# Kernel optimization log

Measured on AMD Instinct MI355X. Metric: run time of the kernel, lower is better.

The kernel has to match this reference:

```python
import jax, jax.numpy as jnp
import numpy as np

REG = 0.1
NITER = 30
EPS = 1e-10

def _encode(x, W1, b1, W2, b2):
    # (B, N, D) -> (B, N, H), MLP applied pointwise
    h = jax.nn.relu(jnp.einsum('bnd,dh->bnh', x, W1) + b1)
    return jnp.einsum('bnh,he->bne', h, W2) + b2

def _l2_normalize(x):
    n = jnp.linalg.norm(x, axis=-1, keepdims=True)
    return x / jnp.maximum(n, 1e-12)

def setup_inputs() -> dict:
    key = jax.random.key(0)
    ks = jax.random.split(key, 6)
    B, N, D, H, E = 32, 1024, 128, 512, 256
    A_batch = jax.random.normal(ks[0], (B, N, D), dtype=jnp.float32)
    B_batch = jax.random.normal(ks[1], (B, N, D), dtype=jnp.float32)
    mask = jnp.ones((B, N), dtype=bool)
    W1 = jax.random.normal(ks[2], (D, H), dtype=jnp.float32) * (1.0 / np.sqrt(D))
    b1 = jnp.zeros((H,), dtype=jnp.float32)
    W2 = jax.random.normal(ks[3], (H, E), dtype=jnp.float32) * (1.0 / np.sqrt(H))
    b2 = jnp.zeros((E,), dtype=jnp.float32)
    return {"A_batch": A_batch, "B_batch": B_batch, "mask": mask,
            "W1": W1, "b1": b1, "W2": W2, "b2": b2}

def reference(A_batch, B_batch, mask, W1, b1, W2, b2):
    A_emb = _l2_normalize(_encode(A_batch, W1, b1, W2, b2))  # (B,N,E)
    B_emb = _l2_normalize(_encode(B_batch, W1, b1, W2, b2))  # (B,M,E)
    C = 1.0 - jnp.einsum('bne,bme->bnm', A_emb, B_emb)       # (B,N,M)
    K = jnp.exp(-C / REG)
    m = mask.astype(jnp.float32)                             # (B,N)
    lengths = m.sum(axis=1)[:, None, None]                   # (B,1,1)
    u_target = m[:, :, None] / lengths                       # (B,N,1)
    v_target = m[:, :, None] / lengths                       # (B,M,1)
    K = K * (m[:, :, None] * m[:, None, :])                  # masked kernel

    def body(_, uv):
        u, v = uv
        u = u_target / (jnp.einsum('bnm,bmk->bnk', K, v) + EPS)
        v = v_target / (jnp.einsum('bnm,bnk->bmk', K, u) + EPS)
        return (u, v)

    u, v = jax.lax.fori_loop(0, NITER, body, (u_target, v_target))
    T = u * K * jnp.swapaxes(v, 1, 2)                        # (B,N,M)
    cost = jnp.sum(T * C, axis=(1, 2))                       # (B,)
    return cost
```

## Files before the change

kernel.cpp:

```cpp
#include <hip/hip_runtime.h>
#include <hip/hip_bf16.h>

namespace {
constexpr int NB = 32;
constexpr int NN = 1024;
constexpr int ND = 128;
constexpr int NH = 512;
constexpr int NE = 256;
constexpr float FEPS = 1e-10f;
}

typedef short bf16x8v __attribute__((ext_vector_type(8)));
typedef unsigned short u16x8 __attribute__((ext_vector_type(8)));
typedef float f32x4 __attribute__((ext_vector_type(4)));
typedef float f32x2 __attribute__((ext_vector_type(2)));

__device__ __forceinline__ unsigned short bf16_rne(float x) {
  unsigned int u = __float_as_uint(x);
  u += 0x7FFFu + ((u >> 16) & 1u);
  return (unsigned short)(u >> 16);
}
__device__ __forceinline__ float bf2f(unsigned short h) {
  return __uint_as_float((unsigned int)h << 16);
}

__device__ __forceinline__ unsigned char f2f8(float x) {
  unsigned short u = __builtin_bit_cast(unsigned short, (_Float16)x);
  u = (unsigned short)(u + 0x7Fu + ((u >> 8) & 1u));
  return (unsigned char)(u >> 8);
}
__device__ __forceinline__ float f8tof(unsigned int b) {
  return (float)__builtin_bit_cast(_Float16, (unsigned short)(b << 8));
}

#if __has_builtin(__builtin_amdgcn_cvt_pk_f32_bf8)
#define DEC8(DST, D) {                                                          \
    f32x2 p_;                                                                   \
    p_ = __builtin_amdgcn_cvt_pk_f32_bf8((int)(D).x, false); (DST)[0] = p_.x; (DST)[1] = p_.y; \
    p_ = __builtin_amdgcn_cvt_pk_f32_bf8((int)(D).x, true);  (DST)[2] = p_.x; (DST)[3] = p_.y; \
    p_ = __builtin_amdgcn_cvt_pk_f32_bf8((int)(D).y, false); (DST)[4] = p_.x; (DST)[5] = p_.y; \
    p_ = __builtin_amdgcn_cvt_pk_f32_bf8((int)(D).y, true);  (DST)[6] = p_.x; (DST)[7] = p_.y; \
  }
#else
#define DEC8(DST, D) {                                                          \
    (DST)[0] = f8tof((D).x & 255u);         (DST)[1] = f8tof(((D).x >> 8) & 255u);  \
    (DST)[2] = f8tof(((D).x >> 16) & 255u); (DST)[3] = f8tof((D).x >> 24);          \
    (DST)[4] = f8tof((D).y & 255u);         (DST)[5] = f8tof(((D).y >> 8) & 255u);  \
    (DST)[6] = f8tof(((D).y >> 16) & 255u); (DST)[7] = f8tof((D).y >> 24);          \
  }
#endif

__global__ void k_prep_w(const float* __restrict__ W1, const float* __restrict__ W2,
                         unsigned short* __restrict__ W1f, unsigned short* __restrict__ W2f,
                         float* __restrict__ zbase)
{
  const int t = blockIdx.x * blockDim.x + threadIdx.x;
  for (int i = t; i < 31 * NB * NN; i += 768 * 256) zbase[i] = 0.f;

  if (t < 128 * 512) {
    const int j = t & 7, l = (t >> 3) & 63, ks = (t >> 9) & 3, ct = t >> 11;
    const int k = ks * 32 + ((l >> 4) << 3) + j;
    const int n = (ct << 4) + (l & 15);
    W1f[t] = bf16_rne(W1[k * NH + n]);
  } else {
    const int t2 = t - 128 * 512;
    const int j = t2 & 7, l = (t2 >> 3) & 63, ks = (t2 >> 9) & 15, ct = t2 >> 13;
    const int k = ks * 32 + ((l >> 4) << 3) + j;
    const int n = (ct << 4) + (l & 15);
    W2f[t2] = bf16_rne(W2[k * NE + n]);
  }
}

__global__ __launch_bounds__(256) void k_encode_mfma(
    const float* __restrict__ Ain, const float* __restrict__ Bin,
    const unsigned short* __restrict__ W1f, const float* __restrict__ b1,
    const unsigned short* __restrict__ W2f, const float* __restrict__ b2,
    unsigned short* __restrict__ Aemb, unsigned short* __restrict__ Bemb)
{
  __shared__ __align__(16) char smem[81920];
  const int tid = threadIdx.x;
  const int lane = tid & 63;
  const int w = tid >> 6;
  const int g0 = blockIdx.x * 64;
  const float* src; unsigned short* dst; int r0;
  if (g0 < NB * NN) { src = Ain; dst = Aemb; r0 = g0; }
  else              { src = Bin; dst = Bemb; r0 = g0 - NB * NN; }

  {
    const int row = tid >> 2;
    const int q = tid & 3;
    const float* xr = src + (size_t)(r0 + row) * ND + q * 32;
    const int rx = (row & 7) << 4;
#pragma unroll
    for (int uq = 0; uq < 4; ++uq) {
      const float4 f0 = *(const float4*)(xr + uq * 8);
      const float4 f1 = *(const float4*)(xr + uq * 8 + 4);
      u16x8 p;
      p[0] = bf16_rne(f0.x); p[1] = bf16_rne(f0.y); p[2] = bf16_rne(f0.z); p[3] = bf16_rne(f0.w);
      p[4] = bf16_rne(f1.x); p[5] = bf16_rne(f1.y); p[6] = bf16_rne(f1.z); p[7] = bf16_rne(f1.w);
      const int byte = (row * 256 + q * 64 + uq * 16) ^ rx;
      *(u16x8*)(smem + byte) = p;
    }
  }
  __syncthreads();

  bf16x8v xa[4];
  {
    const int r = w * 16 + (lane & 15);
    const int rx = (r & 7) << 4;
#pragma unroll
    for (int ks = 0; ks < 4; ++ks) {
      const int byte = (r * 256 + ks * 64 + ((lane >> 4) << 4)) ^ rx;
      xa[ks] = *(const bf16x8v*)(smem + byte);
    }
  }

  const bf16x8v* W1v = (const bf16x8v*)W1f;
  const bf16x8v* W2v = (const bf16x8v*)W2f;
  char* Hbase = smem + 16384;

#pragma unroll
  for (int ct = 0; ct < 32; ct += 2) {
    f32x4 a0 = {0.f, 0.f, 0.f, 0.f};
    f32x4 a1 = {0.f, 0.f, 0.f, 0.f};
#pragma unroll
    for (int ks = 0; ks < 4; ++ks) {
      const bf16x8v wb0 = W1v[((ct << 2) + ks) * 64 + lane];
      const bf16x8v wb1 = W1v[(((ct + 1) << 2) + ks) * 64 + lane];
      a0 = __builtin_amdgcn_mfma_f32_16x16x32_bf16(xa[ks], wb0, a0, 0, 0, 0);
      a1 = __builtin_amdgcn_mfma_f32_16x16x32_bf16(xa[ks], wb1, a1, 0, 0, 0);
    }
    const int c0 = (ct << 4) + (lane & 15);
    const float bv0 = b1[c0];
    const float bv1 = b1[c0 + 16];
    const int rbase = w * 16 + ((lane >> 4) << 2);
#pragma unroll
    for (int reg = 0; reg < 4; ++reg) {
      const int r = rbase + reg;
      const int rx = (r & 7) << 4;
      const float h0 = fmaxf(a0[reg] + bv0, 0.f);
      const float h1 = fmaxf(a1[reg] + bv1, 0.f);
      *(unsigned short*)(Hbase + ((r * 1024 + c0 * 2) ^ rx)) = bf16_rne(h0);
      *(unsigned short*)(Hbase + ((r * 1024 + (c0 + 16) * 2) ^ rx)) = bf16_rne(h1);
    }
  }
  __syncthreads();

  bf16x8v ha[16];
  {
    const int r = w * 16 + (lane & 15);
    const int rx = (r & 7) << 4;
#pragma unroll
    for (int ks = 0; ks < 16; ++ks) {
      const int byte = (r * 1024 + ks * 64 + ((lane >> 4) << 4)) ^ rx;
      ha[ks] = *(const bf16x8v*)(Hbase + byte);
    }
  }

  f32x4 acc[16];
#pragma unroll
  for (int ct = 0; ct < 16; ct += 2) {
    f32x4 a0 = {0.f, 0.f, 0.f, 0.f};
    f32x4 a1 = {0.f, 0.f, 0.f, 0.f};
#pragma unroll
    for (int ks = 0; ks < 16; ++ks) {
      const bf16x8v wb0 = W2v[((ct << 4) + ks) * 64 + lane];
      const bf16x8v wb1 = W2v[(((ct + 1) << 4) + ks) * 64 + lane];
      a0 = __builtin_amdgcn_mfma_f32_16x16x32_bf16(ha[ks], wb0, a0, 0, 0, 0);
      a1 = __builtin_amdgcn_mfma_f32_16x16x32_bf16(ha[ks], wb1, a1, 0, 0, 0);
    }
    acc[ct] = a0;
    acc[ct + 1] = a1;
  }

  float ss[4] = {0.f, 0.f, 0.f, 0.f};
#pragma unroll
  for (int ct = 0; ct < 16; ++ct) {
    const float bv = b2[(ct << 4) + (lane & 15)];
#pragma unroll
    for (int reg = 0; reg < 4; ++reg) {
      const float e = acc[ct][reg] + bv;
      acc[ct][reg] = e;
      ss[reg] += e * e;
    }
  }
#pragma unroll
  for (int reg = 0; reg < 4; ++reg) {
#pragma unroll
    for (int m = 1; m < 16; m <<= 1) ss[reg] += __shfl_xor(ss[reg], m);
    ss[reg] = 1.f / fmaxf(sqrtf(ss[reg]), 1e-12f);
  }
  {
    const int rbase = r0 + w * 16 + ((lane >> 4) << 2);
    const int cbase = lane & 15;
#pragma unroll
    for (int ct = 0; ct < 16; ++ct) {
#pragma unroll
      for (int reg = 0; reg < 4; ++reg) {
        dst[(size_t)(rbase + reg) * NE + (ct << 4) + cbase] = bf16_rne(acc[ct][reg] * ss[reg]);
      }
    }
  }
}

__global__ __launch_bounds__(256) void k_gram_mfma(
    const unsigned short* __restrict__ Aemb, const unsigned short* __restrict__ Bemb,
    unsigned char* __restrict__ Km)
{
  __shared__ __align__(16) char smem[16384];
  const int b = blockIdx.z;
  const int m0 = blockIdx.x * 128;
  const int n0 = blockIdx.y * 128;
  const int tid = threadIdx.x;
  const int lane = tid & 63;
  const int w = tid >> 6;

  const unsigned short* Ap = Aemb + ((size_t)b * NN + n0) * NE;
  const unsigned short* Bp = Bemb + ((size_t)b * NN + m0) * NE;

  f32x4 acc[2][8];
#pragma unroll
  for (int nt = 0; nt < 2; ++nt)
#pragma unroll
    for (int mt = 0; mt < 8; ++mt) acc[nt][mt] = (f32x4){0.f, 0.f, 0.f, 0.f};

  const int sr = tid >> 1;
  const int kh = (tid & 1) * 16;
  const int rxs = (sr & 7) << 4;
  const int koff = (lane >> 4) << 4;

  for (int kc = 0; kc < 8; ++kc) {
    __syncthreads();
    const u16x8 av0 = *(const u16x8*)(Ap + (size_t)sr * NE + kc * 32 + kh);
    const u16x8 av1 = *(const u16x8*)(Ap + (size_t)sr * NE + kc * 32 + kh + 8);
    const u16x8 bv0 = *(const u16x8*)(Bp + (size_t)sr * NE + kc * 32 + kh);
    const u16x8 bv1 = *(const u16x8*)(Bp + (size_t)sr * NE + kc * 32 + kh + 8);
    *(u16x8*)(smem + ((sr * 64 + kh * 2) ^ rxs)) = av0;
    *(u16x8*)(smem + ((sr * 64 + kh * 2 + 16) ^ rxs)) = av1;
    *(u16x8*)(smem + 8192 + ((sr * 64 + kh * 2) ^ rxs)) = bv0;
    *(u16x8*)(smem + 8192 + ((sr * 64 + kh * 2 + 16) ^ rxs)) = bv1;
    __syncthreads();

    bf16x8v af[2], bfm[8];
#pragma unroll
    for (int nt = 0; nt < 2; ++nt) {
      const int r = w * 32 + nt * 16 + (lane & 15);
      af[nt] = *(const bf16x8v*)(smem + ((r * 64 + koff) ^ ((r & 7) << 4)));
    }
#pragma unroll
    for (int mt = 0; mt < 8; ++mt) {
      const int r = mt * 16 + (lane & 15);
      bfm[mt] = *(const bf16x8v*)(smem + 8192 + ((r * 64 + koff) ^ ((r & 7) << 4)));
    }
#pragma unroll
    for (int nt = 0; nt < 2; ++nt)
#pragma unroll
      for (int mt = 0; mt < 8; ++mt)
        acc[nt][mt] = __builtin_amdgcn_mfma_f32_16x16x32_bf16(af[nt], bfm[mt], acc[nt][mt], 0, 0, 0);
  }

  const int mcol = lane & 15;
  const int rbase = (lane >> 4) << 2;
#pragma unroll
  for (int nt = 0; nt < 2; ++nt) {
#pragma unroll
    for (int reg = 0; reg < 4; ++reg) {
      const int n = n0 + w * 32 + nt * 16 + rbase + reg;
      unsigned char* Kp = Km + ((size_t)b * NN + n) * NN + m0 + mcol;
#pragma unroll
      for (int mt = 0; mt < 8; ++mt) {
        const float s = acc[nt][mt][reg];
        Kp[mt * 16] = f2f8(__expf((s - 1.f) * 10.f));
      }
    }
  }
}

#define VV_FROM(CPTR) {                                                          \
    const float4 c0 = *(const float4*)((CPTR) + lane * 8);                       \
    const float4 c1 = *(const float4*)((CPTR) + lane * 8 + 4);                   \
    const float4 c2 = *(const float4*)((CPTR) + 512 + lane * 8);                 \
    const float4 c3 = *(const float4*)((CPTR) + 512 + lane * 8 + 4);             \
    vv[0] = __fdividef(vt, c0.x + FEPS);  vv[1] = __fdividef(vt, c0.y + FEPS);   \
    vv[2] = __fdividef(vt, c0.z + FEPS);  vv[3] = __fdividef(vt, c0.w + FEPS);   \
    vv[4] = __fdividef(vt, c1.x + FEPS);  vv[5] = __fdividef(vt, c1.y + FEPS);   \
    vv[6] = __fdividef(vt, c1.z + FEPS);  vv[7] = __fdividef(vt, c1.w + FEPS);   \
    vv[8] = __fdividef(vt, c2.x + FEPS);  vv[9] = __fdividef(vt, c2.y + FEPS);   \
    vv[10] = __fdividef(vt, c2.z + FEPS); vv[11] = __fdividef(vt, c2.w + FEPS);  \
    vv[12] = __fdividef(vt, c3.x + FEPS); vv[13] = __fdividef(vt, c3.y + FEPS);  \
    vv[14] = __fdividef(vt, c3.z + FEPS); vv[15] = __fdividef(vt, c3.w + FEPS);  \
  }

#define CW_REDUCE(ARR, DST) {                                                    \
    _Pragma("unroll") for (int j = 0; j < 8; ++j) {                              \
      cw[w][lane * 8 + j] = ARR[j];                                              \
      cw[w][512 + lane * 8 + j] = ARR[8 + j];                                    \
    }                                                                            \
    __syncthreads();                                                             \
    const int e0 = tid * 4;                                                      \
    float4 s0 = *(const float4*)&cw[0][e0];                                      \
    const float4 s1 = *(const float4*)&cw[1][e0];                                \
    const float4 s2 = *(const float4*)&cw[2][e0];                                \
    const float4 s3 = *(const float4*)&cw[3][e0];                                \
    s0.x += s1.x + s2.x + s3.x;                                                  \
    s0.y += s1.y + s2.y + s3.y;                                                  \
    s0.z += s1.z + s2.z + s3.z;                                                  \
    s0.w += s1.w + s2.w + s3.w;                                                  \
    float* cn = (DST) + b * NN + e0;                                             \
    atomicAdd(cn + 0, s0.x);                                                     \
    atomicAdd(cn + 1, s0.y);                                                     \
    atomicAdd(cn + 2, s0.z);                                                     \
    atomicAdd(cn + 3, s0.w);                                                     \
  }

__global__ __launch_bounds__(256) void k_sink_it(
    const unsigned char* __restrict__ Km, const float* __restrict__ csumprev,
    float* __restrict__ csumnext)
{
  __shared__ float cw[4][1024];
  const int b = blockIdx.x >> 4;
  const int rb = blockIdx.x & 15;
  const int tid = threadIdx.x;
  const int w = tid >> 6, lane = tid & 63;
  const float vt = 1.f / NN;

  float vv[16];
  if (csumprev) {
    const float* cp = csumprev + b * NN;
    VV_FROM(cp)
  } else {
#pragma unroll
    for (int j = 0; j < 16; ++j) vv[j] = vt;
  }

  const int row0 = rb * 64 + w * 16;
  const unsigned char* Kbase = Km + ((size_t)b * NN + row0) * NN;

  uint2 kr[32];
#pragma unroll
  for (int r = 0; r < 16; ++r) {
    kr[2 * r]     = *(const uint2*)(Kbase + (size_t)r * NN + lane * 8);
    kr[2 * r + 1] = *(const uint2*)(Kbase + (size_t)r * NN + 512 + lane * 8);
  }

  float s[16];
#pragma unroll
  for (int r = 0; r < 16; ++r) {
    float kf[16];
    DEC8(kf, kr[2 * r])
    DEC8(kf + 8, kr[2 * r + 1])
    float a = 0.f;
#pragma unroll
    for (int j = 0; j < 16; ++j) a += kf[j] * vv[j];
    s[r] = a;
  }
#pragma unroll
  for (int m = 1; m < 64; m <<= 1) {
#pragma unroll
    for (int r = 0; r < 16; ++r) s[r] += __shfl_xor(s[r], m);
  }

  float ca[16];
#pragma unroll
  for (int j = 0; j < 16; ++j) ca[j] = 0.f;
#pragma unroll
  for (int r = 0; r < 16; ++r) {
    const float u = __fdividef(vt, s[r] + FEPS);
    float kf[16];
    DEC8(kf, kr[2 * r])
    DEC8(kf + 8, kr[2 * r + 1])
#pragma unroll
    for (int j = 0; j < 16; ++j) ca[j] += kf[j] * u;
  }

  CW_REDUCE(ca, csumnext)
}

__global__ __launch_bounds__(256) void k_sink_last(
    const unsigned char* __restrict__ Km, const float* __restrict__ csumprev,
    float* __restrict__ csumnext, float* __restrict__ tcol)
{
  __shared__ float cw[4][1024];
  const int b = blockIdx.x >> 5;
  const int rb = blockIdx.x & 31;
  const int tid = threadIdx.x;
  const int w = tid >> 6, lane = tid & 63;
  const float vt = 1.f / NN;

  float vv[16];
  {
    const float* cp = csumprev + b * NN;
    VV_FROM(cp)
  }

  const int row0 = rb * 32 + w * 8;
  const unsigned char* Kbase = Km + ((size_t)b * NN + row0) * NN;

  uint2 kr[16];
#pragma unroll
  for (int r = 0; r < 8; ++r) {
    kr[2 * r]     = *(const uint2*)(Kbase + (size_t)r * NN + lane * 8);
    kr[2 * r + 1] = *(const uint2*)(Kbase + (size_t)r * NN + 512 + lane * 8);
  }

  float s[8];
#pragma unroll
  for (int r = 0; r < 8; ++r) {
    float kf[16];
    DEC8(kf, kr[2 * r])
    DEC8(kf + 8, kr[2 * r + 1])
    float a = 0.f;
#pragma unroll
    for (int j = 0; j < 16; ++j) a += kf[j] * vv[j];
    s[r] = a;
  }
#pragma unroll
  for (int m = 1; m < 64; m <<= 1) {
#pragma unroll
    for (int r = 0; r < 8; ++r) s[r] += __shfl_xor(s[r], m);
  }

  float ca[16], cc[16];
#pragma unroll
  for (int j = 0; j < 16; ++j) { ca[j] = 0.f; cc[j] = 0.f; }
#pragma unroll
  for (int r = 0; r < 8; ++r) {
    const float u = __fdividef(vt, s[r] + FEPS);
    float kf[16];
    DEC8(kf, kr[2 * r])
    DEC8(kf + 8, kr[2 * r + 1])
#pragma unroll
    for (int j = 0; j < 16; ++j) {
      const float t = kf[j] * u;
      ca[j] += t;
      const float lk = (kf[j] > 0.f) ? __logf(kf[j]) : 0.f;
      cc[j] += t * lk;
    }
  }

  CW_REDUCE(ca, csumnext)
  __syncthreads();
  CW_REDUCE(cc, tcol)
}

__global__ __launch_bounds__(256) void k_cost_final(
    const float* __restrict__ csumlast, const float* __restrict__ tcol,
    float* __restrict__ out)
{
  __shared__ float red[4];
  const int b = blockIdx.x;
  const int tid = threadIdx.x;
  const int w = tid >> 6, lane = tid & 63;
  const float vt = 1.f / NN;

  const float4 c = *(const float4*)(csumlast + b * NN + tid * 4);
  const float4 t = *(const float4*)(tcol + b * NN + tid * 4);
  float s = t.x * __fdividef(vt, c.x + FEPS)
          + t.y * __fdividef(vt, c.y + FEPS)
          + t.z * __fdividef(vt, c.z + FEPS)
          + t.w * __fdividef(vt, c.w + FEPS);
#pragma unroll
  for (int m = 1; m < 64; m <<= 1) s += __shfl_xor(s, m);
  if (lane == 0) red[w] = s;
  __syncthreads();
  if (tid == 0) out[b] = -0.1f * (red[0] + red[1] + red[2] + red[3]);
}

extern "C" void kernel_launch(void* const* d_in, const int* in_sizes, int n_in,
                              void* d_out, int out_size, void* d_ws, size_t ws_size,
                              hipStream_t stream)
{
  const float* A  = (const float*)d_in[0];
  const float* Bx = (const float*)d_in[1];
  const float* W1 = (const float*)d_in[3];
  const float* b1 = (const float*)d_in[4];
  const float* W2 = (const float*)d_in[5];
  const float* b2 = (const float*)d_in[6];
  float* out = (float*)d_out;

  float* csumbuf = (float*)d_ws;
  float* tcol    = csumbuf + 30 * NB * NN;
  unsigned short* W1f  = (unsigned short*)(tcol + NB * NN);
  unsigned short* W2f  = W1f + 128 * 512;
  unsigned short* Aemb = W2f + 512 * 256;
  unsigned short* Bemb = Aemb + (size_t)NB * NN * NE;
  unsigned char*  Km   = (unsigned char*)(Bemb + (size_t)NB * NN * NE);

  k_prep_w<<<768, 256, 0, stream>>>(W1, W2, W1f, W2f, csumbuf);
  k_encode_mfma<<<1024, 256, 0, stream>>>(A, Bx, W1f, b1, W2f, b2, Aemb, Bemb);
  k_gram_mfma<<<dim3(8, 8, NB), 256, 0, stream>>>(Aemb, Bemb, Km);

  for (int it = 0; it < 29; ++it) {
    k_sink_it<<<512, 256, 0, stream>>>(
        Km, it == 0 ? (const float*)nullptr : csumbuf + (size_t)(it - 1) * NB * NN,
        csumbuf + (size_t)it * NB * NN);
  }
  k_sink_last<<<1024, 256, 0, stream>>>(Km, csumbuf + (size_t)28 * NB * NN,
                                        csumbuf + (size_t)29 * NB * NN, tcol);
  k_cost_final<<<NB, 256, 0, stream>>>(csumbuf + (size_t)29 * NB * NN, tcol, out);
}
```

Baseline: 507.6 us.

## Stage MLP weights through LDS with register prefetch; widen K loads to 16 bytes

The encoder kernel now stages W1 and W2 weight tiles through shared memory. Each tile is prefetched into registers one step ahead and shared by all waves, replacing per-wave global loads of the same weights. The W2 loop is restructured to split the K dimension across two accumulators per column tile, which adds a barrier per tile. The Sinkhorn kernels now load each lane's 16 contiguous fp8 K values with a single 128-bit load instead of two 64-bit loads, and the column-vector indexing and reductions are remapped to match.

```diff
diff --git a/kernel.cpp b/kernel.cpp
--- a/kernel.cpp
+++ b/kernel.cpp
@@ -34,21 +34,19 @@
 }
 
 #if __has_builtin(__builtin_amdgcn_cvt_pk_f32_bf8)
-#define DEC8(DST, D) {                                                          \
+#define DEC8(DST, W) {                                                          \
     f32x2 p_;                                                                   \
-    p_ = __builtin_amdgcn_cvt_pk_f32_bf8((int)(D).x, false); (DST)[0] = p_.x; (DST)[1] = p_.y; \
-    p_ = __builtin_amdgcn_cvt_pk_f32_bf8((int)(D).x, true);  (DST)[2] = p_.x; (DST)[3] = p_.y; \
-    p_ = __builtin_amdgcn_cvt_pk_f32_bf8((int)(D).y, false); (DST)[4] = p_.x; (DST)[5] = p_.y; \
-    p_ = __builtin_amdgcn_cvt_pk_f32_bf8((int)(D).y, true);  (DST)[6] = p_.x; (DST)[7] = p_.y; \
+    p_ = __builtin_amdgcn_cvt_pk_f32_bf8((int)(W), false); (DST)[0] = p_.x; (DST)[1] = p_.y; \
+    p_ = __builtin_amdgcn_cvt_pk_f32_bf8((int)(W), true);  (DST)[2] = p_.x; (DST)[3] = p_.y; \
   }
 #else
-#define DEC8(DST, D) {                                                          \
-    (DST)[0] = f8tof((D).x & 255u);         (DST)[1] = f8tof(((D).x >> 8) & 255u);  \
-    (DST)[2] = f8tof(((D).x >> 16) & 255u); (DST)[3] = f8tof((D).x >> 24);          \
-    (DST)[4] = f8tof((D).y & 255u);         (DST)[5] = f8tof(((D).y >> 8) & 255u);  \
-    (DST)[6] = f8tof(((D).y >> 16) & 255u); (DST)[7] = f8tof((D).y >> 24);          \
+#define DEC8(DST, W) {                                                          \
+    (DST)[0] = f8tof((W) & 255u);         (DST)[1] = f8tof(((W) >> 8) & 255u);  \
+    (DST)[2] = f8tof(((W) >> 16) & 255u); (DST)[3] = f8tof((W) >> 24);          \
   }
 #endif
+
+#define DEC16(DST, Q) { DEC8(DST, (Q).x) DEC8((DST) + 4, (Q).y) DEC8((DST) + 8, (Q).z) DEC8((DST) + 12, (Q).w) }
 
 __global__ void k_prep_w(const float* __restrict__ W1, const float* __restrict__ W2,
                          unsigned short* __restrict__ W1f, unsigned short* __restrict__ W2f,
@@ -115,21 +113,37 @@
     }
   }
 
-  const bf16x8v* W1v = (const bf16x8v*)W1f;
-  const bf16x8v* W2v = (const bf16x8v*)W2f;
+  const char* W1b = (const char*)W1f;
+  const char* W2b = (const char*)W2f;
   char* Hbase = smem + 16384;
 
-#pragma unroll
-  for (int ct = 0; ct < 32; ct += 2) {
+  u16x8 rw1[2];
+#pragma unroll
+  for (int p = 0; p < 2; ++p)
+    rw1[p] = *(const u16x8*)(W1b + p * 4096 + tid * 16);
+  __syncthreads();
+
+  for (int cp = 0; cp < 16; ++cp) {
+#pragma unroll
+    for (int p = 0; p < 2; ++p)
+      *(u16x8*)(smem + p * 4096 + tid * 16) = rw1[p];
+    __syncthreads();
+    if (cp < 15) {
+#pragma unroll
+      for (int p = 0; p < 2; ++p)
+        rw1[p] = *(const u16x8*)(W1b + (cp + 1) * 8192 + p * 4096 + tid * 16);
+    }
+
     f32x4 a0 = {0.f, 0.f, 0.f, 0.f};
     f32x4 a1 = {0.f, 0.f, 0.f, 0.f};
 #pragma unroll
     for (int ks = 0; ks < 4; ++ks) {
-      const bf16x8v wb0 = W1v[((ct << 2) + ks) * 64 + lane];
-      const bf16x8v wb1 = W1v[(((ct + 1) << 2) + ks) * 64 + lane];
+      const bf16x8v wb0 = *(const bf16x8v*)(smem + (ks * 64 + lane) * 16);
+      const bf16x8v wb1 = *(const bf16x8v*)(smem + ((4 + ks) * 64 + lane) * 16);
       a0 = __builtin_amdgcn_mfma_f32_16x16x32_bf16(xa[ks], wb0, a0, 0, 0, 0);
       a1 = __builtin_amdgcn_mfma_f32_16x16x32_bf16(xa[ks], wb1, a1, 0, 0, 0);
     }
+    const int ct = cp * 2;
     const int c0 = (ct << 4) + (lane & 15);
     const float bv0 = b1[c0];
     const float bv1 = b1[c0 + 16];
@@ -143,8 +157,8 @@
       *(unsigned short*)(Hbase + ((r * 1024 + c0 * 2) ^ rx)) = bf16_rne(h0);
       *(unsigned short*)(Hbase + ((r * 1024 + (c0 + 16) * 2) ^ rx)) = bf16_rne(h1);
     }
-  }
-  __syncthreads();
+    __syncthreads();
+  }
 
   bf16x8v ha[16];
   {
@@ -157,20 +171,35 @@
     }
   }
 
+  u16x8 rw2[4];
+#pragma unroll
+  for (int p = 0; p < 4; ++p)
+    rw2[p] = *(const u16x8*)(W2b + p * 4096 + tid * 16);
+
   f32x4 acc[16];
-#pragma unroll
-  for (int ct = 0; ct < 16; ct += 2) {
+  for (int ct = 0; ct < 16; ++ct) {
+#pragma unroll
+    for (int p = 0; p < 4; ++p)
+      *(u16x8*)(smem + p * 4096 + tid * 16) = rw2[p];
+    __syncthreads();
+    if (ct < 15) {
+#pragma unroll
+      for (int p = 0; p < 4; ++p)
+        rw2[p] = *(const u16x8*)(W2b + (ct + 1) * 16384 + p * 4096 + tid * 16);
+    }
+
     f32x4 a0 = {0.f, 0.f, 0.f, 0.f};
     f32x4 a1 = {0.f, 0.f, 0.f, 0.f};
 #pragma unroll
-    for (int ks = 0; ks < 16; ++ks) {
-      const bf16x8v wb0 = W2v[((ct << 4) + ks) * 64 + lane];
-      const bf16x8v wb1 = W2v[(((ct + 1) << 4) + ks) * 64 + lane];
+    for (int ks = 0; ks < 8; ++ks) {
+      const bf16x8v wb0 = *(const bf16x8v*)(smem + (ks * 64 + lane) * 16);
+      const bf16x8v wb1 = *(const bf16x8v*)(smem + ((8 + ks) * 64 + lane) * 16);
       a0 = __builtin_amdgcn_mfma_f32_16x16x32_bf16(ha[ks], wb0, a0, 0, 0, 0);
-      a1 = __builtin_amdgcn_mfma_f32_16x16x32_bf16(ha[ks], wb1, a1, 0, 0, 0);
-    }
-    acc[ct] = a0;
-    acc[ct + 1] = a1;
+      a1 = __builtin_amdgcn_mfma_f32_16x16x32_bf16(ha[8 + ks], wb1, a1, 0, 0, 0);
+    }
+    acc[ct][0] = a0[0] + a1[0]; acc[ct][1] = a0[1] + a1[1];
+    acc[ct][2] = a0[2] + a1[2]; acc[ct][3] = a0[3] + a1[3];
+    __syncthreads();
   }
 
   float ss[4] = {0.f, 0.f, 0.f, 0.f};
@@ -277,10 +306,10 @@
 }
 
 #define VV_FROM(CPTR) {                                                          \
-    const float4 c0 = *(const float4*)((CPTR) + lane * 8);                       \
-    const float4 c1 = *(const float4*)((CPTR) + lane * 8 + 4);                   \
-    const float4 c2 = *(const float4*)((CPTR) + 512 + lane * 8);                 \
-    const float4 c3 = *(const float4*)((CPTR) + 512 + lane * 8 + 4);             \
+    const float4 c0 = *(const float4*)((CPTR) + lane * 16);                      \
+    const float4 c1 = *(const float4*)((CPTR) + lane * 16 + 4);                  \
+    const float4 c2 = *(const float4*)((CPTR) + lane * 16 + 8);                  \
+    const float4 c3 = *(const float4*)((CPTR) + lane * 16 + 12);                 \
     vv[0] = __fdividef(vt, c0.x + FEPS);  vv[1] = __fdividef(vt, c0.y + FEPS);   \
     vv[2] = __fdividef(vt, c0.z + FEPS);  vv[3] = __fdividef(vt, c0.w + FEPS);   \
     vv[4] = __fdividef(vt, c1.x + FEPS);  vv[5] = __fdividef(vt, c1.y + FEPS);   \
@@ -292,9 +321,8 @@
   }
 
 #define CW_REDUCE(ARR, DST) {                                                    \
-    _Pragma("unroll") for (int j = 0; j < 8; ++j) {                              \
-      cw[w][lane * 8 + j] = ARR[j];                                              \
-      cw[w][512 + lane * 8 + j] = ARR[8 + j];                                    \
+    _Pragma("unroll") for (int j = 0; j < 16; ++j) {                             \
+      cw[w][lane * 16 + j] = ARR[j];                                             \
     }                                                                            \
     __syncthreads();                                                             \
     const int e0 = tid * 4;                                                      \
@@ -334,21 +362,18 @@
   }
 
   const int row0 = rb * 64 + w * 16;
-  const unsigned char* Kbase = Km + ((size_t)b * NN + row0) * NN;
-
-  uint2 kr[32];
-#pragma unroll
-  for (int r = 0; r < 16; ++r) {
-    kr[2 * r]     = *(const uint2*)(Kbase + (size_t)r * NN + lane * 8);
-    kr[2 * r + 1] = *(const uint2*)(Kbase + (size_t)r * NN + 512 + lane * 8);
-  }
+  const unsigned char* Kbase = Km + ((size_t)b * NN + row0) * NN + lane * 16;
+
+  uint4 kr[16];
+#pragma unroll
+  for (int r = 0; r < 16; ++r)
+    kr[r] = *(const uint4*)(Kbase + (size_t)r * NN);
 
   float s[16];
 #pragma unroll
   for (int r = 0; r < 16; ++r) {
     float kf[16];
-    DEC8(kf, kr[2 * r])
-    DEC8(kf + 8, kr[2 * r + 1])
+    DEC16(kf, kr[r])
     float a = 0.f;
 #pragma unroll
     for (int j = 0; j < 16; ++j) a += kf[j] * vv[j];
@@ -367,8 +392,7 @@
   for (int r = 0; r < 16; ++r) {
     const float u = __fdividef(vt, s[r] + FEPS);
     float kf[16];
-    DEC8(kf, kr[2 * r])
-    DEC8(kf + 8, kr[2 * r + 1])
+    DEC16(kf, kr[r])
 #pragma unroll
     for (int j = 0; j < 16; ++j) ca[j] += kf[j] * u;
   }
@@ -394,21 +418,18 @@
   }
 
   const int row0 = rb * 32 + w * 8;
-  const unsigned char* Kbase = Km + ((size_t)b * NN + row0) * NN;
-
-  uint2 kr[16];
-#pragma unroll
-  for (int r = 0; r < 8; ++r) {
-    kr[2 * r]     = *(const uint2*)(Kbase + (size_t)r * NN + lane * 8);
-    kr[2 * r + 1] = *(const uint2*)(Kbase + (size_t)r * NN + 512 + lane * 8);
-  }
+  const unsigned char* Kbase = Km + ((size_t)b * NN + row0) * NN + lane * 16;
+
+  uint4 kr[8];
+#pragma unroll
+  for (int r = 0; r < 8; ++r)
+    kr[r] = *(const uint4*)(Kbase + (size_t)r * NN);
 
   float s[8];
 #pragma unroll
   for (int r = 0; r < 8; ++r) {
     float kf[16];
-    DEC8(kf, kr[2 * r])
-    DEC8(kf + 8, kr[2 * r + 1])
+    DEC16(kf, kr[r])
     float a = 0.f;
 #pragma unroll
     for (int j = 0; j < 16; ++j) a += kf[j] * vv[j];
@@ -427,8 +448,7 @@
   for (int r = 0; r < 8; ++r) {
     const float u = __fdividef(vt, s[r] + FEPS);
     float kf[16];
-    DEC8(kf, kr[2 * r])
-    DEC8(kf + 8, kr[2 * r + 1])
+    DEC16(kf, kr[r])
 #pragma unroll
     for (int j = 0; j < 16; ++j) {
       const float t = kf[j] * u;
```

Measured after the change: 495.3 us. -2.4%, faster.
